# Optimization experiments

Measured on AMD Instinct MI355X. Metric: run time of the kernel, lower is better.

## Reference

```python
import jax, jax.numpy as jnp
import numpy as np
import math

EMBED = 1024
HEADS = 16
HEAD_DIM = 64
HIDDEN = 4 * EMBED
EPS = 1e-5


def setup_inputs() -> dict:
    key = jax.random.key(0)
    ks = jax.random.split(key, 12)
    B, T, C = 2, 2048, EMBED
    s = 0.02
    return {
        "x": jax.random.normal(ks[0], (B, T, C), jnp.float32),
        "ln1_g": jnp.ones((C,), jnp.float32),
        "ln1_b": jnp.zeros((C,), jnp.float32),
        "qkv_w": jax.random.normal(ks[1], (C, 3 * C), jnp.float32) * s,
        "qkv_b": jnp.zeros((3 * C,), jnp.float32),
        "out_w": jax.random.normal(ks[2], (C, C), jnp.float32) * s,
        "out_b": jnp.zeros((C,), jnp.float32),
        "ln2_g": jnp.ones((C,), jnp.float32),
        "ln2_b": jnp.zeros((C,), jnp.float32),
        "fc1_w": jax.random.normal(ks[3], (C, HIDDEN), jnp.float32) * s,
        "fc1_b": jnp.zeros((HIDDEN,), jnp.float32),
        "fc2_w": jax.random.normal(ks[4], (HIDDEN, C), jnp.float32) * s,
        "fc2_b": jnp.zeros((C,), jnp.float32),
    }


def _layernorm(x, g, b):
    mu = jnp.mean(x, axis=-1, keepdims=True)
    var = jnp.var(x, axis=-1, keepdims=True)
    return (x - mu) * jax.lax.rsqrt(var + EPS) * g + b


def _attention(x, qkv_w, qkv_b, out_w, out_b):
    B, T, C = x.shape
    qkv = x @ qkv_w + qkv_b  # [B,T,3C]
    q, k, v = jnp.split(qkv, 3, axis=-1)
    # [B,H,T,hd]
    def heads(t):
        return t.reshape(B, T, HEADS, HEAD_DIM).transpose(0, 2, 1, 3)
    q, k, v = heads(q), heads(k), heads(v)
    scale = 1.0 / math.sqrt(HEAD_DIM)
    attn = jnp.einsum('bhqd,bhkd->bhqk', q, k) * scale
    causal = jnp.triu(jnp.ones((T, T), bool), k=1)
    attn = jnp.where(causal, -jnp.inf, attn)
    attn = jax.nn.softmax(attn, axis=-1)
    out = jnp.einsum('bhqk,bhkd->bhqd', attn, v)
    out = out.transpose(0, 2, 1, 3).reshape(B, T, C)
    return out @ out_w + out_b


def reference(x, ln1_g, ln1_b, qkv_w, qkv_b, out_w, out_b, ln2_g, ln2_b, fc1_w, fc1_b, fc2_w, fc2_b):
    x = x + _attention(_layernorm(x, ln1_g, ln1_b), qkv_w, qkv_b, out_w, out_b)
    h = _layernorm(x, ln2_g, ln2_b)
    h = jax.nn.gelu(h @ fc1_w + fc1_b, approximate=False) @ fc2_w + fc2_b
    return x + h
```

## Files before the change

kernel.cpp:

```cpp
#include <hip/hip_runtime.h>
#include <hip/hip_bf16.h>
#include <math.h>

typedef float f32x4 __attribute__((ext_vector_type(4)));
typedef __bf16 bf16x8 __attribute__((ext_vector_type(8)));
typedef __hip_bfloat16 bf16;

constexpr int T_SEQ = 2048;
constexpr int C_EMB = 1024;
constexpr int N_HEAD = 16;
constexpr int D_HEAD = 64;
constexpr int BATCH = 2;
constexpr int M_ROWS = BATCH * T_SEQ;
constexpr int HIDDEN_DIM = 4096;

static __device__ __forceinline__ f32x4 zero4() {
  f32x4 z; z[0] = 0.f; z[1] = 0.f; z[2] = 0.f; z[3] = 0.f; return z;
}

static __device__ __forceinline__ void gl_lds16(const bf16* g, bf16* l) {
  __builtin_amdgcn_global_load_lds(
      (const __attribute__((address_space(1))) unsigned int*)g,
      (__attribute__((address_space(3))) unsigned int*)l, 16, 0, 0);
}

#define BAR() asm volatile("s_barrier" ::: "memory")

__global__ __launch_bounds__(256) void ln_kernel(const float* __restrict__ x,
                                                 const float* __restrict__ gamma,
                                                 const float* __restrict__ beta,
                                                 bf16* __restrict__ out) {
  int row = blockIdx.x;
  const float* xr = x + (size_t)row * C_EMB;
  int t = threadIdx.x;
  float4 v = *(const float4*)&xr[t * 4];
  float s = v.x + v.y + v.z + v.w;
  float ss = v.x * v.x + v.y * v.y + v.z * v.z + v.w * v.w;
#pragma unroll
  for (int off = 32; off > 0; off >>= 1) {
    s += __shfl_down(s, off, 64);
    ss += __shfl_down(ss, off, 64);
  }
  __shared__ float sbuf[8];
  int w = t >> 6;
  if ((t & 63) == 0) { sbuf[w] = s; sbuf[4 + w] = ss; }
  __syncthreads();
  s = sbuf[0] + sbuf[1] + sbuf[2] + sbuf[3];
  ss = sbuf[4] + sbuf[5] + sbuf[6] + sbuf[7];
  float mu = s * (1.0f / C_EMB);
  float var = ss * (1.0f / C_EMB) - mu * mu;
  float rstd = rsqrtf(var + 1e-5f);
  float4 g4 = *(const float4*)&gamma[t * 4];
  float4 b4 = *(const float4*)&beta[t * 4];
  bf16* orow = out + (size_t)row * C_EMB + t * 4;
  orow[0] = __float2bfloat16((v.x - mu) * rstd * g4.x + b4.x);
  orow[1] = __float2bfloat16((v.y - mu) * rstd * g4.y + b4.y);
  orow[2] = __float2bfloat16((v.z - mu) * rstd * g4.z + b4.z);
  orow[3] = __float2bfloat16((v.w - mu) * rstd * g4.w + b4.w);
}

__global__ __launch_bounds__(256) void ln_red(const float* __restrict__ p0,
                                              const float* __restrict__ p1,
                                              const float* __restrict__ bias,
                                              const float* __restrict__ res,
                                              const float* __restrict__ gamma,
                                              const float* __restrict__ beta,
                                              float* __restrict__ x2,
                                              bf16* __restrict__ xb) {
  int row = blockIdx.x;
  int t = threadIdx.x;
  size_t base = (size_t)row * C_EMB + t * 4;
  float4 a = *(const float4*)&p0[base];
  float4 b = *(const float4*)&p1[base];
  float4 r = *(const float4*)&res[base];
  float4 bi = *(const float4*)&bias[t * 4];
  float4 v;
  v.x = a.x + b.x + r.x + bi.x;
  v.y = a.y + b.y + r.y + bi.y;
  v.z = a.z + b.z + r.z + bi.z;
  v.w = a.w + b.w + r.w + bi.w;
  *(float4*)&x2[base] = v;
  float s = v.x + v.y + v.z + v.w;
  float ss = v.x * v.x + v.y * v.y + v.z * v.z + v.w * v.w;
#pragma unroll
  for (int off = 32; off > 0; off >>= 1) {
    s += __shfl_down(s, off, 64);
    ss += __shfl_down(ss, off, 64);
  }
  __shared__ float sbuf[8];
  int w = t >> 6;
  if ((t & 63) == 0) { sbuf[w] = s; sbuf[4 + w] = ss; }
  __syncthreads();
  s = sbuf[0] + sbuf[1] + sbuf[2] + sbuf[3];
  ss = sbuf[4] + sbuf[5] + sbuf[6] + sbuf[7];
  float mu = s * (1.0f / C_EMB);
  float var = ss * (1.0f / C_EMB) - mu * mu;
  float rstd = rsqrtf(var + 1e-5f);
  float4 g4 = *(const float4*)&gamma[t * 4];
  float4 b4 = *(const float4*)&beta[t * 4];
  bf16* orow = xb + base;
  orow[0] = __float2bfloat16((v.x - mu) * rstd * g4.x + b4.x);
  orow[1] = __float2bfloat16((v.y - mu) * rstd * g4.y + b4.y);
  orow[2] = __float2bfloat16((v.z - mu) * rstd * g4.z + b4.z);
  orow[3] = __float2bfloat16((v.w - mu) * rstd * g4.w + b4.w);
}

__global__ __launch_bounds__(256) void cast_transpose(const float* __restrict__ src,
                                                      bf16* __restrict__ dst,
                                                      int K, int N) {
  __shared__ float tile[32][33];
  int n0 = blockIdx.x * 32, k0 = blockIdx.y * 32;
  int tx = threadIdx.x & 31, ty = threadIdx.x >> 5;
#pragma unroll
  for (int i = 0; i < 4; ++i)
    tile[ty + 8 * i][tx] = src[(size_t)(k0 + ty + 8 * i) * N + n0 + tx];
  __syncthreads();
#pragma unroll
  for (int i = 0; i < 4; ++i)
    dst[(size_t)(n0 + ty + 8 * i) * K + k0 + tx] = __float2bfloat16(tile[tx][ty + 8 * i]);
}

__global__ __launch_bounds__(256) void transpose_v(const bf16* __restrict__ V,
                                                   bf16* __restrict__ Vt) {
  int tt = blockIdx.x, bh = blockIdx.y;
  __shared__ bf16 tile[64][72];
  const bf16* src = V + ((size_t)bh * T_SEQ + tt * 64) * 64;
  int t = threadIdx.x;
  for (int idx = t; idx < 512; idx += 256) {
    int r = idx >> 3, c = (idx & 7) * 8;
    *(int4*)&tile[r][c] = *(const int4*)&src[r * 64 + c];
  }
  __syncthreads();
  bf16* dst = Vt + ((size_t)bh * 64) * T_SEQ + tt * 64;
  for (int idx = t; idx < 512; idx += 256) {
    int d = idx >> 3, c = (idx & 7) * 8;
    union { bf16 h[8]; int4 v; } u;
#pragma unroll
    for (int j = 0; j < 8; ++j) u.h[j] = tile[c + j][d];
    *(int4*)&dst[(size_t)d * T_SEQ + c] = u.v;
  }
}

template <int EPI>
__global__ __launch_bounds__(512) void gemm8p(
    const bf16* __restrict__ A, const bf16* __restrict__ Bt,
    const float* __restrict__ bias, int M, int N, int K,
    bf16* __restrict__ out_b16,
    bf16* __restrict__ q_out, bf16* __restrict__ k_out, bf16* __restrict__ v_out) {
  constexpr int NFR = 4;
  __shared__ bf16 Asl[2][2][128 * 64];
  __shared__ bf16 Bsl[2][2][128 * 64];

  int gx = gridDim.x, nwg = gx * gridDim.y;
  int flat = blockIdx.y * gx + blockIdx.x;
  int swz = (flat & 7) * (nwg >> 3) + (flat >> 3);
  int bx = swz % gx, by = swz / gx;

  int m0 = by * 256, n0 = bx * 256;
  int t = threadIdx.x;
  int wv = t >> 6, lane = t & 63, g = lane >> 4, r16 = lane & 15;
  int wm = wv >> 2, wn = wv & 3;

  f32x4 acc[8][NFR];
#pragma unroll
  for (int i = 0; i < 8; ++i)
#pragma unroll
    for (int j = 0; j < NFR; ++j) acc[i][j] = zero4();

  int lrow8 = lane >> 3;
  int srcg = (lane & 7) ^ lrow8;
  int NT = K / 64;

  auto stageA = [&](int tile, int h) {
    int par = tile & 1;
    const bf16* base = A + (size_t)(m0 + h * 128) * K + tile * 64;
#pragma unroll
    for (int j = 0; j < 2; ++j) {
      const bf16* src = base + (size_t)((wv * 2 + j) * 8 + lrow8) * K + srcg * 8;
      gl_lds16(src, &Asl[par][h][((wv * 2 + j) * 8) * 64]);
    }
  };
  auto stageB = [&](int tile, int h) {
    int par = tile & 1;
    const bf16* base = Bt + (size_t)(n0 + h * 128) * K + tile * 64;
#pragma unroll
    for (int j = 0; j < 2; ++j) {
      const bf16* src = base + (size_t)((wv * 2 + j) * 8 + lrow8) * K + srcg * 8;
      gl_lds16(src, &Bsl[par][h][((wv * 2 + j) * 8) * 64]);
    }
  };

  int xk[2];
#pragma unroll
  for (int kk = 0; kk < 2; ++kk) xk[kk] = (((kk * 4 + g) ^ (r16 & 7)) << 3);
  int bhalf = wn >> 1;
  int blrow0 = (wn & 1) * 64;

  stageA(0, 0); stageA(0, 1); stageB(0, 0); stageB(0, 1);
  if (NT > 1) {
    stageB(1, 0); stageB(1, 1);
    asm volatile("s_waitcnt vmcnt(4)" ::: "memory");
  } else {
    asm volatile("s_waitcnt vmcnt(0)" ::: "memory");
  }
  BAR();

  bf16x8 bfr[NFR][2];

  for (int u = 0; u < NT; ++u) {
    int par = u & 1;
    const bf16* Ab = &Asl[par][wm][0];
    const bf16* Bb = &Bsl[par][bhalf][0];
#pragma unroll
    for (int q = 0; q < 4; ++q) {
      if (q == 0) {
#pragma unroll
        for (int ni = 0; ni < NFR; ++ni)
#pragma unroll
          for (int kk = 0; kk < 2; ++kk)
            bfr[ni][kk] = *(const bf16x8*)&Bb[(blrow0 + ni * 16 + r16) * 64 + xk[kk]];
      }
      bf16x8 af[2][2];
#pragma unroll
      for (int d = 0; d < 2; ++d)
#pragma unroll
        for (int kk = 0; kk < 2; ++kk)
          af[d][kk] = *(const bf16x8*)&Ab[((2 * q + d) * 16 + r16) * 64 + xk[kk]];
      if (q == 0) { if (u + 1 < NT) stageA(u + 1, 0); }
      else if (q == 1) { if (u + 1 < NT) stageA(u + 1, 1); }
      else if (q == 2) { if (u + 2 < NT) stageB(u + 2, 0); }
      else { if (u + 2 < NT) stageB(u + 2, 1); }
      BAR();
      asm volatile("s_waitcnt lgkmcnt(0)" ::: "memory");
      __builtin_amdgcn_sched_barrier(0);
      __builtin_amdgcn_s_setprio(1);
#pragma unroll
      for (int d = 0; d < 2; ++d)
#pragma unroll
        for (int ni = 0; ni < NFR; ++ni) {
          acc[2 * q + d][ni] = __builtin_amdgcn_mfma_f32_16x16x32_bf16(af[d][0], bfr[ni][0], acc[2 * q + d][ni], 0, 0, 0);
          acc[2 * q + d][ni] = __builtin_amdgcn_mfma_f32_16x16x32_bf16(af[d][1], bfr[ni][1], acc[2 * q + d][ni], 0, 0, 0);
        }
      __builtin_amdgcn_s_setprio(0);
      if (q == 3) {
        if (u + 2 < NT)
          asm volatile("s_waitcnt vmcnt(4)" ::: "memory");
        else
          asm volatile("s_waitcnt vmcnt(0)" ::: "memory");
      }
      BAR();
    }
  }

#pragma unroll
  for (int mi = 0; mi < 8; ++mi) {
#pragma unroll
    for (int ni = 0; ni < NFR; ++ni) {
      int col = n0 + wn * 64 + ni * 16 + r16;
      float bv = bias[col];
#pragma unroll
      for (int reg = 0; reg < 4; ++reg) {
        int row = m0 + wm * 128 + mi * 16 + g * 4 + reg;
        float v = acc[mi][ni][reg] + bv;
        if constexpr (EPI == 0) {
          int part = col >> 10, cc = col & 1023;
          int hh = cc >> 6, dd = cc & 63;
          int bb = row >> 11, tt2 = row & 2047;
          size_t idx = (((size_t)bb * N_HEAD + hh) * T_SEQ + tt2) * D_HEAD + dd;
          if (part == 0) q_out[idx] = __float2bfloat16(v * 0.125f);
          else if (part == 1) k_out[idx] = __float2bfloat16(v);
          else v_out[idx] = __float2bfloat16(v);
        } else {
          float ge = 0.5f * v * (1.0f + erff(v * 0.70710678118f));
          out_b16[(size_t)row * N + col] = __float2bfloat16(ge);
        }
      }
    }
  }
}

template <int EPI, int BN>
__global__ __launch_bounds__(512) void gemm256(
    const bf16* __restrict__ A, const bf16* __restrict__ Bt,
    const float* __restrict__ bias, int M, int N, int K, int ksplit,
    bf16* __restrict__ out_b16,
    float* __restrict__ part0, float* __restrict__ part1) {
  constexpr int NFR = BN / 64;
  constexpr int NB = BN / 64;
  __shared__ bf16 Abuf[2][256 * 64];
  __shared__ bf16 Bbuf[2][BN * 64];

  int gx = gridDim.x, nwg = gx * gridDim.y;
  int flat = blockIdx.y * gx + blockIdx.x;
  int swz = (flat & 7) * (nwg >> 3) + (flat >> 3);
  int bx = swz % gx, by = swz / gx;

  int m0 = by * 256, n0 = bx * BN;
  int t = threadIdx.x;
  int wv = t >> 6, lane = t & 63, g = lane >> 4, r16 = lane & 15;
  int wm = wv >> 2, wn = wv & 3;

  f32x4 acc[8][NFR];
#pragma unroll
  for (int i = 0; i < 8; ++i)
#pragma unroll
    for (int j = 0; j < NFR; ++j) acc[i][j] = zero4();

  int srow = wv * 8 + (lane >> 3);
  int srcg = (lane & 7) ^ (lane >> 3);

  int klen = K / ksplit;
  int kbeg = blockIdx.z * klen;
  int NT = klen / 64;

  const bf16* gAp[4];
  const bf16* gBp[NB];
#pragma unroll
  for (int i = 0; i < 4; ++i)
    gAp[i] = A + (size_t)(m0 + i * 64 + srow) * K + kbeg + srcg * 8;
#pragma unroll
  for (int i = 0; i < NB; ++i)
    gBp[i] = Bt + (size_t)(n0 + i * 64 + srow) * K + kbeg + srcg * 8;

  int aoff[8], boff[NFR], xk[2];
#pragma unroll
  for (int mi = 0; mi < 8; ++mi) aoff[mi] = (wm * 128 + mi * 16 + r16) * 64;
#pragma unroll
  for (int ni = 0; ni < NFR; ++ni) boff[ni] = (wn * NFR * 16 + ni * 16 + r16) * 64;
#pragma unroll
  for (int kk = 0; kk < 2; ++kk) xk[kk] = (((kk * 4 + g) ^ (r16 & 7)) << 3);

  auto stage = [&](int buf) {
#pragma unroll
    for (int i = 0; i < 4; ++i) {
      gl_lds16(gAp[i], &Abuf[buf][(i * 64 + wv * 8) * 64]);
      gAp[i] += 64;
    }
#pragma unroll
    for (int i = 0; i < NB; ++i) {
      gl_lds16(gBp[i], &Bbuf[buf][(i * 64 + wv * 8) * 64]);
      gBp[i] += 64;
    }
  };

  auto compute = [&](int buf) {
    const bf16* Ab = &Abuf[buf][0];
    const bf16* Bb = &Bbuf[buf][0];
    bf16x8 bfr[NFR][2];
#pragma unroll
    for (int ni = 0; ni < NFR; ++ni)
#pragma unroll
      for (int kk = 0; kk < 2; ++kk)
        bfr[ni][kk] = *(const bf16x8*)&Bb[boff[ni] + xk[kk]];
    bf16x8 aa[2][2];
#pragma unroll
    for (int kk = 0; kk < 2; ++kk) aa[0][kk] = *(const bf16x8*)&Ab[aoff[0] + xk[kk]];
#pragma unroll
    for (int mi = 0; mi < 8; ++mi) {
      if (mi + 1 < 8) {
#pragma unroll
        for (int kk = 0; kk < 2; ++kk)
          aa[(mi + 1) & 1][kk] = *(const bf16x8*)&Ab[aoff[mi + 1] + xk[kk]];
      }
#pragma unroll
      for (int ni = 0; ni < NFR; ++ni) {
        acc[mi][ni] = __builtin_amdgcn_mfma_f32_16x16x32_bf16(aa[mi & 1][0], bfr[ni][0], acc[mi][ni], 0, 0, 0);
        acc[mi][ni] = __builtin_amdgcn_mfma_f32_16x16x32_bf16(aa[mi & 1][1], bfr[ni][1], acc[mi][ni], 0, 0, 0);
      }
    }
  };

  stage(0);
  __syncthreads();
  for (int tt = 0; tt < NT; ++tt) {
    int cur = tt & 1;
    if (tt + 1 < NT) stage(cur ^ 1);
    compute(cur);
    __syncthreads();
  }

  float* pout = (blockIdx.z == 0) ? part0 : part1;

#pragma unroll
  for (int mi = 0; mi < 8; ++mi) {
#pragma unroll
    for (int ni = 0; ni < NFR; ++ni) {
      int col = n0 + wn * NFR * 16 + ni * 16 + r16;
#pragma unroll
      for (int reg = 0; reg < 4; ++reg) {
        int row = m0 + wm * 128 + mi * 16 + g * 4 + reg;
        pout[(size_t)row * N + col] = acc[mi][ni][reg];
      }
    }
  }
  (void)bias; (void)out_b16;
}

__global__ __launch_bounds__(256) void reduce_add(const float* __restrict__ p0,
                                                  const float* __restrict__ p1,
                                                  const float* __restrict__ bias,
                                                  const float* __restrict__ res,
                                                  float* __restrict__ out,
                                                  int total, int N) {
  for (int i = (blockIdx.x * 256 + threadIdx.x) * 4; i < total; i += gridDim.x * 1024) {
    float4 a = *(const float4*)&p0[i];
    float4 b = *(const float4*)&p1[i];
    float4 r = *(const float4*)&res[i];
    float4 bi = *(const float4*)&bias[i & (N - 1)];
    float4 o;
    o.x = a.x + b.x + r.x + bi.x;
    o.y = a.y + b.y + r.y + bi.y;
    o.z = a.z + b.z + r.z + bi.z;
    o.w = a.w + b.w + r.w + bi.w;
    *(float4*)&out[i] = o;
  }
}

__global__ __launch_bounds__(256) void attn_kernel(const bf16* __restrict__ Q,
                                                   const bf16* __restrict__ Kg,
                                                   const bf16* __restrict__ Vt,
                                                   bf16* __restrict__ O) {
  constexpr int NQ = T_SEQ / 64;
  int p = blockIdx.x, bh = blockIdx.y;
  int qtA = p, qtB = NQ - 1 - p;
  int b = bh >> 4, h = bh & 15;
  __shared__ bf16 Ks[2][64 * 64];
  __shared__ bf16 Vs[2][64 * 64];
  __shared__ bf16 Ps[4][16 * 64];
  int t = threadIdx.x, w = t >> 6, lane = t & 63, g = lane >> 4, r16 = lane & 15;

  const bf16* QpA = Q + ((size_t)bh * T_SEQ + qtA * 64) * 64;
  const bf16* QpB = Q + ((size_t)bh * T_SEQ + qtB * 64) * 64;
  bf16x8 qfA[2], qfB[2];
#pragma unroll
  for (int kk = 0; kk < 2; ++kk) {
    qfA[kk] = *(const bf16x8*)&QpA[(w * 16 + r16) * 64 + kk * 32 + g * 8];
    qfB[kk] = *(const bf16x8*)&QpB[(w * 16 + r16) * 64 + kk * 32 + g * 8];
  }

  float lsA[4] = {0.f, 0.f, 0.f, 0.f}, lsB[4] = {0.f, 0.f, 0.f, 0.f};
  f32x4 oA[4], oB[4];
#pragma unroll
  for (int i = 0; i < 4; ++i) { oA[i] = zero4(); oB[i] = zero4(); }

  bf16* Psw = Ps[w];

  int sg0 = w * 128 + lane, sg1 = w * 128 + 64 + lane;
  int sr0 = sg0 >> 3, sc0 = (sg0 & 7) ^ (sr0 & 7);
  int sr1 = sg1 >> 3, sc1 = (sg1 & 7) ^ (sr1 & 7);

  auto stage = [&](int kt, int buf) {
    const bf16* Kp = Kg + ((size_t)bh * T_SEQ + kt * 64) * 64;
    const bf16* Vp = Vt + (size_t)bh * 64 * T_SEQ + kt * 64;
    gl_lds16(Kp + sr0 * 64 + sc0 * 8, &Ks[buf][(w * 128) * 8]);
    gl_lds16(Vp + (size_t)sr0 * T_SEQ + sc0 * 8, &Vs[buf][(w * 128) * 8]);
    gl_lds16(Kp + sr1 * 64 + sc1 * 8, &Ks[buf][(w * 128 + 64) * 8]);
    gl_lds16(Vp + (size_t)sr1 * T_SEQ + sc1 * 8, &Vs[buf][(w * 128 + 64) * 8]);
  };

  auto process = [&](const bf16x8* qf, float* ls, f32x4* o_acc, bool diag,
                     const bf16* Ksb, const bf16* Vsb) {
    f32x4 s[4];
#pragma unroll
    for (int ni = 0; ni < 4; ++ni) {
      s[ni] = zero4();
#pragma unroll
      for (int kk = 0; kk < 2; ++kk) {
        bf16x8 kf = *(const bf16x8*)&Ksb[(ni * 16 + r16) * 64 + (((kk * 4 + g) ^ (r16 & 7)) << 3)];
        s[ni] = __builtin_amdgcn_mfma_f32_16x16x32_bf16(qf[kk], kf, s[ni], 0, 0, 0);
      }
    }
    if (diag) {
#pragma unroll
      for (int ni = 0; ni < 4; ++ni) {
        int kl = ni * 16 + r16;
#pragma unroll
        for (int reg = 0; reg < 4; ++reg) {
          int ql = w * 16 + g * 4 + reg;
          if (kl > ql) s[ni][reg] = -1e30f;
        }
      }
    }
#pragma unroll
    for (int ni = 0; ni < 4; ++ni) {
#pragma unroll
      for (int reg = 0; reg < 4; ++reg) {
        float pv = __expf(s[ni][reg]);
        s[ni][reg] = pv;
        ls[reg] += pv;
        int rr = g * 4 + reg;
        Psw[rr * 64 + (((ni * 2 + (r16 >> 3)) ^ (rr & 7)) << 3) + (r16 & 7)] =
            __float2bfloat16(pv);
      }
    }
    bf16x8 pf[2];
#pragma unroll
    for (int kk = 0; kk < 2; ++kk)
      pf[kk] = *(const bf16x8*)&Psw[r16 * 64 + (((kk * 4 + g) ^ (r16 & 7)) << 3)];
#pragma unroll
    for (int nd = 0; nd < 4; ++nd)
#pragma unroll
      for (int kk = 0; kk < 2; ++kk) {
        bf16x8 vf = *(const bf16x8*)&Vsb[(nd * 16 + r16) * 64 + (((kk * 4 + g) ^ (r16 & 7)) << 3)];
        o_acc[nd] = __builtin_amdgcn_mfma_f32_16x16x32_bf16(pf[kk], vf, o_acc[nd], 0, 0, 0);
      }
  };

  stage(0, 0);
  __syncthreads();
  for (int kt = 0; kt <= qtB; ++kt) {
    int cur = kt & 1;
    if (kt + 1 <= qtB) stage(kt + 1, cur ^ 1);
    process(qfB, lsB, oB, kt == qtB, &Ks[cur][0], &Vs[cur][0]);
    if (kt <= qtA) process(qfA, lsA, oA, kt == qtA, &Ks[cur][0], &Vs[cur][0]);
    __syncthreads();
  }

#pragma unroll
  for (int reg = 0; reg < 4; ++reg) {
#pragma unroll
    for (int off = 1; off < 16; off <<= 1) {
      lsA[reg] += __shfl_xor(lsA[reg], off, 64);
      lsB[reg] += __shfl_xor(lsB[reg], off, 64);
    }
  }
#pragma unroll
  for (int reg = 0; reg < 4; ++reg) {
    float invA = 1.0f / lsA[reg];
    float invB = 1.0f / lsB[reg];
    int rowA = b * T_SEQ + qtA * 64 + w * 16 + g * 4 + reg;
    int rowB = b * T_SEQ + qtB * 64 + w * 16 + g * 4 + reg;
#pragma unroll
    for (int nd = 0; nd < 4; ++nd) {
      int col = h * 64 + nd * 16 + r16;
      O[(size_t)rowA * C_EMB + col] = __float2bfloat16(oA[nd][reg] * invA);
      O[(size_t)rowB * C_EMB + col] = __float2bfloat16(oB[nd][reg] * invB);
    }
  }
}

extern "C" void kernel_launch(void* const* d_in, const int* in_sizes, int n_in,
                              void* d_out, int out_size, void* d_ws, size_t ws_size,
                              hipStream_t stream) {
  (void)in_sizes; (void)n_in; (void)out_size; (void)ws_size;
  const float* x     = (const float*)d_in[0];
  const float* ln1_g = (const float*)d_in[1];
  const float* ln1_b = (const float*)d_in[2];
  const float* qkv_w = (const float*)d_in[3];
  const float* qkv_b = (const float*)d_in[4];
  const float* out_w = (const float*)d_in[5];
  const float* out_b = (const float*)d_in[6];
  const float* ln2_g = (const float*)d_in[7];
  const float* ln2_b = (const float*)d_in[8];
  const float* fc1_w = (const float*)d_in[9];
  const float* fc1_b = (const float*)d_in[10];
  const float* fc2_w = (const float*)d_in[11];
  const float* fc2_b = (const float*)d_in[12];
  float* out = (float*)d_out;

  char* ws = (char*)d_ws;
  size_t off = 0;
  auto alloc = [&](size_t bytes) {
    void* p = ws + off;
    off += (bytes + 255) & ~(size_t)255;
    return p;
  };
  bf16* Wqkv = (bf16*)alloc((size_t)3 * C_EMB * C_EMB * 2);
  bf16* Wout = (bf16*)alloc((size_t)C_EMB * C_EMB * 2);
  bf16* W1   = (bf16*)alloc((size_t)HIDDEN_DIM * C_EMB * 2);
  bf16* W2   = (bf16*)alloc((size_t)C_EMB * HIDDEN_DIM * 2);
  float* x2  = (float*)alloc((size_t)M_ROWS * C_EMB * 4);
  bf16* Xb   = (bf16*)alloc((size_t)M_ROWS * C_EMB * 2);
  bf16* Qb   = (bf16*)alloc((size_t)M_ROWS * C_EMB * 2 * 4);
  bf16* Kb   = Qb + (size_t)M_ROWS * C_EMB;
  bf16* Vb   = Kb + (size_t)M_ROWS * C_EMB;
  bf16* Vtb  = Vb + (size_t)M_ROWS * C_EMB;
  bf16* H1   = Qb;
  float* p0o = (float*)Qb;
  float* p1o = (float*)Vb;
  float* p0f = (float*)Wqkv;
  float* p1f = (float*)alloc((size_t)M_ROWS * C_EMB * 4);

  cast_transpose<<<dim3(3 * C_EMB / 32, C_EMB / 32), 256, 0, stream>>>(qkv_w, Wqkv, C_EMB, 3 * C_EMB);
  cast_transpose<<<dim3(C_EMB / 32, C_EMB / 32), 256, 0, stream>>>(out_w, Wout, C_EMB, C_EMB);
  cast_transpose<<<dim3(HIDDEN_DIM / 32, C_EMB / 32), 256, 0, stream>>>(fc1_w, W1, C_EMB, HIDDEN_DIM);
  cast_transpose<<<dim3(C_EMB / 32, HIDDEN_DIM / 32), 256, 0, stream>>>(fc2_w, W2, HIDDEN_DIM, C_EMB);

  ln_kernel<<<M_ROWS, 256, 0, stream>>>(x, ln1_g, ln1_b, Xb);

  gemm8p<0><<<dim3(3 * C_EMB / 256, M_ROWS / 256), 512, 0, stream>>>(
      Xb, Wqkv, qkv_b, M_ROWS, 3 * C_EMB, C_EMB,
      nullptr, Qb, Kb, Vb);

  transpose_v<<<dim3(T_SEQ / 64, BATCH * N_HEAD), 256, 0, stream>>>(Vb, Vtb);

  attn_kernel<<<dim3(T_SEQ / 128, BATCH * N_HEAD), 256, 0, stream>>>(Qb, Kb, Vtb, Xb);

  gemm256<3, 128><<<dim3(C_EMB / 128, M_ROWS / 256, 2), 512, 0, stream>>>(
      Xb, Wout, nullptr, M_ROWS, C_EMB, C_EMB, 2,
      nullptr, p0o, p1o);
  ln_red<<<M_ROWS, 256, 0, stream>>>(p0o, p1o, out_b, x, ln2_g, ln2_b, x2, Xb);

  gemm8p<2><<<dim3(HIDDEN_DIM / 256, M_ROWS / 256), 512, 0, stream>>>(
      Xb, W1, fc1_b, M_ROWS, HIDDEN_DIM, C_EMB,
      H1, nullptr, nullptr, nullptr);

  gemm256<3, 128><<<dim3(C_EMB / 128, M_ROWS / 256, 2), 512, 0, stream>>>(
      H1, W2, nullptr, M_ROWS, C_EMB, HIDDEN_DIM, 2,
      nullptr, p0f, p1f);
  reduce_add<<<2048, 256, 0, stream>>>(p0f, p1f, fc2_b, x2, out,
                                       M_ROWS * C_EMB, C_EMB);
}
```

Baseline: 246.4 us.

## Replace split-K GEMMs with 128x128 tile GEMM fusing bias and residual

The out-projection and fc2 GEMMs drop split-K with fp32 partial buffers and a separate reduce/LN-reduce pass. A new 128x128-tile GEMM adds bias and residual directly in its epilogue, and the second LayerNorm reuses the plain ln_kernel on x2. The four weight cast-transpose launches are merged into one kernel. This removes the partial-buffer traffic and extra launches, but the non-split GEMMs run longer K loops, and the grid changes from 256 to 256 blocks with a smaller tile.

```diff
diff --git a/kernel.cpp b/kernel.cpp
--- a/kernel.cpp
+++ b/kernel.cpp
@@ -59,57 +59,20 @@
   orow[3] = __float2bfloat16((v.w - mu) * rstd * g4.w + b4.w);
 }
 
-__global__ __launch_bounds__(256) void ln_red(const float* __restrict__ p0,
-                                              const float* __restrict__ p1,
-                                              const float* __restrict__ bias,
-                                              const float* __restrict__ res,
-                                              const float* __restrict__ gamma,
-                                              const float* __restrict__ beta,
-                                              float* __restrict__ x2,
-                                              bf16* __restrict__ xb) {
-  int row = blockIdx.x;
-  int t = threadIdx.x;
-  size_t base = (size_t)row * C_EMB + t * 4;
-  float4 a = *(const float4*)&p0[base];
-  float4 b = *(const float4*)&p1[base];
-  float4 r = *(const float4*)&res[base];
-  float4 bi = *(const float4*)&bias[t * 4];
-  float4 v;
-  v.x = a.x + b.x + r.x + bi.x;
-  v.y = a.y + b.y + r.y + bi.y;
-  v.z = a.z + b.z + r.z + bi.z;
-  v.w = a.w + b.w + r.w + bi.w;
-  *(float4*)&x2[base] = v;
-  float s = v.x + v.y + v.z + v.w;
-  float ss = v.x * v.x + v.y * v.y + v.z * v.z + v.w * v.w;
-#pragma unroll
-  for (int off = 32; off > 0; off >>= 1) {
-    s += __shfl_down(s, off, 64);
-    ss += __shfl_down(ss, off, 64);
-  }
-  __shared__ float sbuf[8];
-  int w = t >> 6;
-  if ((t & 63) == 0) { sbuf[w] = s; sbuf[4 + w] = ss; }
-  __syncthreads();
-  s = sbuf[0] + sbuf[1] + sbuf[2] + sbuf[3];
-  ss = sbuf[4] + sbuf[5] + sbuf[6] + sbuf[7];
-  float mu = s * (1.0f / C_EMB);
-  float var = ss * (1.0f / C_EMB) - mu * mu;
-  float rstd = rsqrtf(var + 1e-5f);
-  float4 g4 = *(const float4*)&gamma[t * 4];
-  float4 b4 = *(const float4*)&beta[t * 4];
-  bf16* orow = xb + base;
-  orow[0] = __float2bfloat16((v.x - mu) * rstd * g4.x + b4.x);
-  orow[1] = __float2bfloat16((v.y - mu) * rstd * g4.y + b4.y);
-  orow[2] = __float2bfloat16((v.z - mu) * rstd * g4.z + b4.z);
-  orow[3] = __float2bfloat16((v.w - mu) * rstd * g4.w + b4.w);
-}
-
-__global__ __launch_bounds__(256) void cast_transpose(const float* __restrict__ src,
-                                                      bf16* __restrict__ dst,
-                                                      int K, int N) {
+__global__ __launch_bounds__(256) void cast_transpose_all(
+    const float* __restrict__ qkv_w, bf16* __restrict__ Wqkv,
+    const float* __restrict__ out_w, bf16* __restrict__ Wout,
+    const float* __restrict__ fc1_w, bf16* __restrict__ W1,
+    const float* __restrict__ fc2_w, bf16* __restrict__ W2) {
+  int id = blockIdx.x;
+  const float* src; bf16* dst; int K, N, tt;
+  if (id < 3072)      { src = qkv_w; dst = Wqkv; K = 1024; N = 3072; tt = id; }
+  else if (id < 4096) { src = out_w; dst = Wout; K = 1024; N = 1024; tt = id - 3072; }
+  else if (id < 8192) { src = fc1_w; dst = W1;   K = 1024; N = 4096; tt = id - 4096; }
+  else                { src = fc2_w; dst = W2;   K = 4096; N = 1024; tt = id - 8192; }
+  int ntx = N >> 5;
+  int n0 = (tt % ntx) * 32, k0 = (tt / ntx) * 32;
   __shared__ float tile[32][33];
-  int n0 = blockIdx.x * 32, k0 = blockIdx.y * 32;
   int tx = threadIdx.x & 31, ty = threadIdx.x >> 5;
 #pragma unroll
   for (int i = 0; i < 4; ++i)
@@ -279,15 +242,16 @@
   }
 }
 
-template <int EPI, int BN>
-__global__ __launch_bounds__(512) void gemm256(
+template <int BM, int BN>
+__global__ __launch_bounds__(512) void gemmD(
     const bf16* __restrict__ A, const bf16* __restrict__ Bt,
-    const float* __restrict__ bias, int M, int N, int K, int ksplit,
-    bf16* __restrict__ out_b16,
-    float* __restrict__ part0, float* __restrict__ part1) {
+    const float* __restrict__ bias, int M, int N, int K,
+    const float* __restrict__ res, float* __restrict__ out_f32) {
+  constexpr int NAM = BM / 32;
   constexpr int NFR = BN / 64;
+  constexpr int NA = BM / 64;
   constexpr int NB = BN / 64;
-  __shared__ bf16 Abuf[2][256 * 64];
+  __shared__ bf16 Abuf[2][BM * 64];
   __shared__ bf16 Bbuf[2][BN * 64];
 
   int gx = gridDim.x, nwg = gx * gridDim.y;
@@ -295,44 +259,41 @@
   int swz = (flat & 7) * (nwg >> 3) + (flat >> 3);
   int bx = swz % gx, by = swz / gx;
 
-  int m0 = by * 256, n0 = bx * BN;
+  int m0 = by * BM, n0 = bx * BN;
   int t = threadIdx.x;
   int wv = t >> 6, lane = t & 63, g = lane >> 4, r16 = lane & 15;
   int wm = wv >> 2, wn = wv & 3;
 
-  f32x4 acc[8][NFR];
-#pragma unroll
-  for (int i = 0; i < 8; ++i)
+  f32x4 acc[NAM][NFR];
+#pragma unroll
+  for (int i = 0; i < NAM; ++i)
 #pragma unroll
     for (int j = 0; j < NFR; ++j) acc[i][j] = zero4();
 
   int srow = wv * 8 + (lane >> 3);
   int srcg = (lane & 7) ^ (lane >> 3);
-
-  int klen = K / ksplit;
-  int kbeg = blockIdx.z * klen;
-  int NT = klen / 64;
-
-  const bf16* gAp[4];
+  int NT = K / 64;
+
+  const bf16* gAp[NA];
   const bf16* gBp[NB];
 #pragma unroll
-  for (int i = 0; i < 4; ++i)
-    gAp[i] = A + (size_t)(m0 + i * 64 + srow) * K + kbeg + srcg * 8;
+  for (int i = 0; i < NA; ++i)
+    gAp[i] = A + (size_t)(m0 + i * 64 + srow) * K + srcg * 8;
 #pragma unroll
   for (int i = 0; i < NB; ++i)
-    gBp[i] = Bt + (size_t)(n0 + i * 64 + srow) * K + kbeg + srcg * 8;
-
-  int aoff[8], boff[NFR], xk[2];
-#pragma unroll
-  for (int mi = 0; mi < 8; ++mi) aoff[mi] = (wm * 128 + mi * 16 + r16) * 64;
-#pragma unroll
-  for (int ni = 0; ni < NFR; ++ni) boff[ni] = (wn * NFR * 16 + ni * 16 + r16) * 64;
+    gBp[i] = Bt + (size_t)(n0 + i * 64 + srow) * K + srcg * 8;
+
+  int aoff[NAM], boff[NFR], xk[2];
+#pragma unroll
+  for (int mi = 0; mi < NAM; ++mi) aoff[mi] = (wm * (BM / 2) + mi * 16 + r16) * 64;
+#pragma unroll
+  for (int ni = 0; ni < NFR; ++ni) boff[ni] = (wn * (BN / 4) + ni * 16 + r16) * 64;
 #pragma unroll
   for (int kk = 0; kk < 2; ++kk) xk[kk] = (((kk * 4 + g) ^ (r16 & 7)) << 3);
 
   auto stage = [&](int buf) {
 #pragma unroll
-    for (int i = 0; i < 4; ++i) {
+    for (int i = 0; i < NA; ++i) {
       gl_lds16(gAp[i], &Abuf[buf][(i * 64 + wv * 8) * 64]);
       gAp[i] += 64;
     }
@@ -356,8 +317,8 @@
 #pragma unroll
     for (int kk = 0; kk < 2; ++kk) aa[0][kk] = *(const bf16x8*)&Ab[aoff[0] + xk[kk]];
 #pragma unroll
-    for (int mi = 0; mi < 8; ++mi) {
-      if (mi + 1 < 8) {
+    for (int mi = 0; mi < NAM; ++mi) {
+      if (mi + 1 < NAM) {
 #pragma unroll
         for (int kk = 0; kk < 2; ++kk)
           aa[(mi + 1) & 1][kk] = *(const bf16x8*)&Ab[aoff[mi + 1] + xk[kk]];
@@ -372,47 +333,26 @@
 
   stage(0);
   __syncthreads();
-  for (int tt = 0; tt < NT; ++tt) {
-    int cur = tt & 1;
-    if (tt + 1 < NT) stage(cur ^ 1);
+  for (int tt2 = 0; tt2 < NT; ++tt2) {
+    int cur = tt2 & 1;
+    if (tt2 + 1 < NT) stage(cur ^ 1);
     compute(cur);
     __syncthreads();
   }
 
-  float* pout = (blockIdx.z == 0) ? part0 : part1;
-
-#pragma unroll
-  for (int mi = 0; mi < 8; ++mi) {
+#pragma unroll
+  for (int mi = 0; mi < NAM; ++mi) {
 #pragma unroll
     for (int ni = 0; ni < NFR; ++ni) {
-      int col = n0 + wn * NFR * 16 + ni * 16 + r16;
+      int col = n0 + wn * (BN / 4) + ni * 16 + r16;
+      float bv = bias[col];
 #pragma unroll
       for (int reg = 0; reg < 4; ++reg) {
-        int row = m0 + wm * 128 + mi * 16 + g * 4 + reg;
-        pout[(size_t)row * N + col] = acc[mi][ni][reg];
-      }
-    }
-  }
-  (void)bias; (void)out_b16;
-}
-
-__global__ __launch_bounds__(256) void reduce_add(const float* __restrict__ p0,
-                                                  const float* __restrict__ p1,
-                                                  const float* __restrict__ bias,
-                                                  const float* __restrict__ res,
-                                                  float* __restrict__ out,
-                                                  int total, int N) {
-  for (int i = (blockIdx.x * 256 + threadIdx.x) * 4; i < total; i += gridDim.x * 1024) {
-    float4 a = *(const float4*)&p0[i];
-    float4 b = *(const float4*)&p1[i];
-    float4 r = *(const float4*)&res[i];
-    float4 bi = *(const float4*)&bias[i & (N - 1)];
-    float4 o;
-    o.x = a.x + b.x + r.x + bi.x;
-    o.y = a.y + b.y + r.y + bi.y;
-    o.z = a.z + b.z + r.z + bi.z;
-    o.w = a.w + b.w + r.w + bi.w;
-    *(float4*)&out[i] = o;
+        int row = m0 + wm * (BM / 2) + mi * 16 + g * 4 + reg;
+        size_t idx = (size_t)row * N + col;
+        out_f32[idx] = acc[mi][ni][reg] + bv + res[idx];
+      }
+    }
   }
 }
 
@@ -576,15 +516,9 @@
   bf16* Vb   = Kb + (size_t)M_ROWS * C_EMB;
   bf16* Vtb  = Vb + (size_t)M_ROWS * C_EMB;
   bf16* H1   = Qb;
-  float* p0o = (float*)Qb;
-  float* p1o = (float*)Vb;
-  float* p0f = (float*)Wqkv;
-  float* p1f = (float*)alloc((size_t)M_ROWS * C_EMB * 4);
-
-  cast_transpose<<<dim3(3 * C_EMB / 32, C_EMB / 32), 256, 0, stream>>>(qkv_w, Wqkv, C_EMB, 3 * C_EMB);
-  cast_transpose<<<dim3(C_EMB / 32, C_EMB / 32), 256, 0, stream>>>(out_w, Wout, C_EMB, C_EMB);
-  cast_transpose<<<dim3(HIDDEN_DIM / 32, C_EMB / 32), 256, 0, stream>>>(fc1_w, W1, C_EMB, HIDDEN_DIM);
-  cast_transpose<<<dim3(C_EMB / 32, HIDDEN_DIM / 32), 256, 0, stream>>>(fc2_w, W2, HIDDEN_DIM, C_EMB);
+
+  cast_transpose_all<<<12288, 256, 0, stream>>>(qkv_w, Wqkv, out_w, Wout,
+                                                fc1_w, W1, fc2_w, W2);
 
   ln_kernel<<<M_ROWS, 256, 0, stream>>>(x, ln1_g, ln1_b, Xb);
 
@@ -596,18 +530,15 @@
 
   attn_kernel<<<dim3(T_SEQ / 128, BATCH * N_HEAD), 256, 0, stream>>>(Qb, Kb, Vtb, Xb);
 
-  gemm256<3, 128><<<dim3(C_EMB / 128, M_ROWS / 256, 2), 512, 0, stream>>>(
-      Xb, Wout, nullptr, M_ROWS, C_EMB, C_EMB, 2,
-      nullptr, p0o, p1o);
-  ln_red<<<M_ROWS, 256, 0, stream>>>(p0o, p1o, out_b, x, ln2_g, ln2_b, x2, Xb);
+  gemmD<128, 128><<<dim3(C_EMB / 128, M_ROWS / 128), 512, 0, stream>>>(
+      Xb, Wout, out_b, M_ROWS, C_EMB, C_EMB, x, x2);
+
+  ln_kernel<<<M_ROWS, 256, 0, stream>>>(x2, ln2_g, ln2_b, Xb);
 
   gemm8p<2><<<dim3(HIDDEN_DIM / 256, M_ROWS / 256), 512, 0, stream>>>(
       Xb, W1, fc1_b, M_ROWS, HIDDEN_DIM, C_EMB,
       H1, nullptr, nullptr, nullptr);
 
-  gemm256<3, 128><<<dim3(C_EMB / 128, M_ROWS / 256, 2), 512, 0, stream>>>(
-      H1, W2, nullptr, M_ROWS, C_EMB, HIDDEN_DIM, 2,
-      nullptr, p0f, p1f);
-  reduce_add<<<2048, 256, 0, stream>>>(p0f, p1f, fc2_b, x2, out,
-                                       M_ROWS * C_EMB, C_EMB);
-}
+  gemmD<128, 128><<<dim3(C_EMB / 128, M_ROWS / 128), 512, 0, stream>>>(
+      H1, W2, fc2_b, M_ROWS, C_EMB, HIDDEN_DIM, x2, out);
+}
```

Measured after the change: 240.8 us. 2.3% less time.
